# Kernel tuning notes

Measured on AMD Instinct MI355X. Metric: run time of the kernel, lower is better.

Reference implementation:

```python
import jax, jax.numpy as jnp
import numpy as np

B, M, S, E, LC, V, HOPS = 16, 2048, 6, 128, 512, 32000, 3
PAD = 1


def setup_inputs() -> dict:
    key = jax.random.key(0)
    ks = jax.random.split(key, 16)
    story = jax.random.randint(ks[0], (B, M, S), 0, V)
    kb_len = jax.random.randint(ks[1], (B,), 0, M - LC)
    conv_len = jax.random.randint(ks[2], (B,), 0, LC)
    hidden = jax.random.normal(ks[3], (1, B, 2 * E), jnp.float32)
    dh_outputs = jax.random.normal(ks[4], (B, LC, E), jnp.float32)
    tf_hidden = jax.random.normal(ks[5], (B, E), jnp.float32)
    query_vector = jax.random.normal(ks[6], (B, E), jnp.float32)
    global_pointer = jax.random.uniform(ks[7], (B, M), jnp.float32)
    C = jax.random.normal(ks[8], (HOPS + 1, V, E), jnp.float32) * 0.1
    C = C.at[:, PAD, :].set(0.0)  # padding_idx row is zero
    s = 0.05
    wA1 = jax.random.normal(ks[9], (2 * E, E), jnp.float32) * s
    bA1 = jnp.zeros((E,), jnp.float32)
    wA2 = jax.random.normal(ks[10], (E, E), jnp.float32) * s
    bA2 = jnp.zeros((E,), jnp.float32)
    wC1 = jax.random.normal(ks[11], (2 * E, E), jnp.float32) * s
    bC1 = jnp.zeros((E,), jnp.float32)
    wC2 = jax.random.normal(ks[12], (E, E), jnp.float32) * s
    bC2 = jnp.zeros((E,), jnp.float32)
    wf = jax.random.normal(ks[13], (2 * E, E), jnp.float32) * s
    bf = jnp.zeros((E,), jnp.float32)
    return dict(story=story, kb_len=kb_len, conv_len=conv_len, hidden=hidden,
                dh_outputs=dh_outputs, tf_hidden=tf_hidden, query_vector=query_vector,
                global_pointer=global_pointer, C=C, wA1=wA1, bA1=bA1, wA2=wA2, bA2=bA2,
                wC1=wC1, bC1=bC1, wC2=wC2, bC2=bC2, wf=wf, bf=bf)


def _lrelu(x):
    return jnp.where(x > 0, x, 0.1 * x)  # LeakyReLU(0.1)


def _mlp(x, w1, b1, w2, b2):
    return _lrelu(x @ w1 + b1) @ w2 + b2


def _add_lm(mem, kb_len, conv_len, dh):
    # mem: [B,M,E]; add dh[bi,:conv_len[bi]] into rows [kb_len, kb_len+conv_len)
    pos = jnp.arange(mem.shape[1])[None, :]            # [1,M]
    idx = pos - kb_len[:, None]                        # [B,M]
    mask = (idx >= 0) & (idx < conv_len[:, None])
    gathered = jnp.take_along_axis(dh, jnp.clip(idx, 0, dh.shape[1] - 1)[..., None], axis=1)
    return mem + jnp.where(mask[..., None], gathered, 0.0)


def reference(story, kb_len, conv_len, hidden, dh_outputs, tf_hidden,
              query_vector, global_pointer, C, wA1, bA1, wA2, bA2,
              wC1, bC1, wC2, bC2, wf, bf):
    # --- load_ent_memory: build m_story_ent (dropout off / eval mode) ---
    u = _lrelu(hidden[0] @ wf + bf)                    # hidden.squeeze(0) -> [B,E]
    tf = jnp.broadcast_to(tf_hidden[:, None, :], (B, M, E))
    m_story = []
    eC = None
    for hop in range(HOPS):
        eA = _add_lm(C[hop][story].sum(2), kb_len, conv_len, dh_outputs)       # [B,M,E]
        eA = _mlp(jnp.concatenate([eA, tf], -1), wA1, bA1, wA2, bA2)
        logit = jnp.einsum('bme,be->bm', eA, u)
        p = jax.nn.softmax(logit, axis=1)
        eC = _add_lm(C[hop + 1][story].sum(2), kb_len, conv_len, dh_outputs)   # [B,M,E]
        eC = _mlp(jnp.concatenate([eC, tf], -1), wC1, bC1, wC2, bC2)
        u = u + jnp.einsum('bme,bm->be', eC, p)
        m_story.append(eA)
    m_story.append(eC)
    # --- forward(query_vector, global_pointer) ---
    uq = query_vector
    gp = global_pointer[..., None]                     # [B,M,1]
    prob_logits = None
    prob_soft = None
    for hop in range(HOPS):
        mA = m_story[hop] * gp
        prob_logits = jnp.einsum('bme,be->bm', mA, uq)
        prob_soft = jax.nn.softmax(prob_logits, axis=1)
        mC = m_story[hop + 1] * gp
        uq = uq + jnp.einsum('bme,bm->be', mC, prob_soft)
    return (prob_soft, prob_logits)
```

## Files before the change

kernel.cpp:

```cpp
#include <hip/hip_runtime.h>
#include <math.h>

#define BB 16
#define MM 2048
#define SS 6
#define EE 128
#define LCC 512
#define VV 32000

typedef __attribute__((ext_vector_type(8))) __bf16 bf16x8;
typedef __attribute__((ext_vector_type(4))) float f32x4;

#define XS_STRIDE 264
#define HS_STRIDE 136

static __device__ inline unsigned short bfbits(float x) {
    __bf16 h = (__bf16)x;
    return __builtin_bit_cast(unsigned short, h);
}

#define N_W1  (256 * 128)
#define N_W2  (128 * 128)
#define N_UQ  (BB * EE)
#define N_PREP (N_W1 + N_W2 + 2 * N_UQ)

__global__ __launch_bounds__(256)
void prep_small(const float* __restrict__ W1, const float* __restrict__ W2,
                __bf16* __restrict__ w1t, __bf16* __restrict__ w2t,
                float* __restrict__ uqA, float* __restrict__ uqB)
{
    int i = blockIdx.x * 256 + threadIdx.x;
    if (i < N_W1) { const int n = i >> 8, k = i & 255; w1t[i] = (__bf16)W1[k * EE + n]; return; }
    i -= N_W1;
    if (i < N_W2) { const int n = i >> 7, k = i & 127; w2t[i] = (__bf16)W2[k * EE + n]; return; }
    i -= N_W2;
    if (i < N_UQ) { uqA[i] = 0.f; return; }
    i -= N_UQ;
    if (i < N_UQ) { uqB[i] = 0.f; }
}

__global__ __launch_bounds__(256)
void embed_mlp_mfma(const int* __restrict__ story,
                    const int* __restrict__ kb_len,
                    const int* __restrict__ conv_len,
                    const float* __restrict__ dh,
                    const float* __restrict__ tf,
                    const float* __restrict__ C,
                    const __bf16* __restrict__ w1t, const float* __restrict__ b1,
                    const __bf16* __restrict__ w2t, const float* __restrict__ b2,
                    const float* __restrict__ gp, const float* __restrict__ query,
                    __bf16* __restrict__ mout, float* __restrict__ lbuf0)
{
    __shared__ __bf16 Xs[32 * XS_STRIDE];
    __shared__ int    sidx[32 * SS];
    __bf16* Hs   = Xs;
    float*  plog = (float*)Xs;

    const int bid  = blockIdx.x;
    const int hop  = bid >> 10;
    const int row0 = (bid & 1023) * 32;
    const int b    = row0 >> 11;
    const int tid  = threadIdx.x;

    const float* Ck = C + (size_t)hop * VV * EE;

    for (int i = tid; i < 32 * SS; i += 256) sidx[i] = story[(size_t)row0 * SS + i];

    const int kb   = kb_len[b];
    const int cl   = conv_len[b];
    const int rgrp = tid >> 5;
    const int e4   = (tid & 31) * 4;
    const float4 tf4 = *(const float4*)&tf[b * EE + e4];
    ushort4 tfp;
    tfp.x = bfbits(tf4.x); tfp.y = bfbits(tf4.y); tfp.z = bfbits(tf4.z); tfp.w = bfbits(tf4.w);
    __syncthreads();

    for (int chunk = 0; chunk < 4; ++chunk) {
        const int r  = chunk * 8 + rgrp;
        const int* si = &sidx[r * SS];
        float4 v[SS];
        #pragma unroll
        for (int s = 0; s < SS; ++s)
            v[s] = *(const float4*)&Ck[(size_t)si[s] * EE + e4];
        const int j = ((row0 + r) & (MM - 1)) - kb;
        float4 acc = {0.f, 0.f, 0.f, 0.f};
        if (j >= 0 && j < cl)
            acc = *(const float4*)&dh[((size_t)b * LCC + j) * EE + e4];
        #pragma unroll
        for (int s = 0; s < SS; ++s) {
            acc.x += v[s].x; acc.y += v[s].y; acc.z += v[s].z; acc.w += v[s].w;
        }
        ushort4 pk;
        pk.x = bfbits(acc.x); pk.y = bfbits(acc.y); pk.z = bfbits(acc.z); pk.w = bfbits(acc.w);
        *(ushort4*)&Xs[r * XS_STRIDE + e4]      = pk;
        *(ushort4*)&Xs[r * XS_STRIDE + EE + e4] = tfp;
    }
    __syncthreads();

    const int w       = tid >> 6;
    const int lane    = tid & 63;
    const int lr      = lane & 15;
    const int lk      = lane >> 4;
    const int colbase = w * 32;

    f32x4 acc1[2][2];
    #pragma unroll
    for (int i = 0; i < 2; ++i)
        #pragma unroll
        for (int j = 0; j < 2; ++j) acc1[i][j] = (f32x4){0.f, 0.f, 0.f, 0.f};

    for (int ks = 0; ks < 8; ++ks) {
        bf16x8 a[2], bw[2];
        #pragma unroll
        for (int mt = 0; mt < 2; ++mt)
            a[mt] = *(const bf16x8*)&Xs[(mt * 16 + lr) * XS_STRIDE + ks * 32 + lk * 8];
        #pragma unroll
        for (int nt = 0; nt < 2; ++nt)
            bw[nt] = *(const bf16x8*)&w1t[(size_t)(colbase + nt * 16 + lr) * 256 + ks * 32 + lk * 8];
        #pragma unroll
        for (int mt = 0; mt < 2; ++mt)
            #pragma unroll
            for (int nt = 0; nt < 2; ++nt)
                acc1[mt][nt] = __builtin_amdgcn_mfma_f32_16x16x32_bf16(a[mt], bw[nt], acc1[mt][nt], 0, 0, 0);
    }
    __syncthreads();
    {
        const float b1v[2] = { b1[colbase + lr], b1[colbase + 16 + lr] };
        #pragma unroll
        for (int mt = 0; mt < 2; ++mt)
            #pragma unroll
            for (int nt = 0; nt < 2; ++nt)
                #pragma unroll
                for (int reg = 0; reg < 4; ++reg) {
                    float h = acc1[mt][nt][reg] + b1v[nt];
                    h = (h > 0.f) ? h : 0.1f * h;
                    Hs[(mt * 16 + lk * 4 + reg) * HS_STRIDE + colbase + nt * 16 + lr] = (__bf16)h;
                }
    }
    __syncthreads();

    f32x4 acc2[2][2];
    #pragma unroll
    for (int i = 0; i < 2; ++i)
        #pragma unroll
        for (int j = 0; j < 2; ++j) acc2[i][j] = (f32x4){0.f, 0.f, 0.f, 0.f};

    for (int ks = 0; ks < 4; ++ks) {
        bf16x8 a[2], bw[2];
        #pragma unroll
        for (int mt = 0; mt < 2; ++mt)
            a[mt] = *(const bf16x8*)&Hs[(mt * 16 + lr) * HS_STRIDE + ks * 32 + lk * 8];
        #pragma unroll
        for (int nt = 0; nt < 2; ++nt)
            bw[nt] = *(const bf16x8*)&w2t[(size_t)(colbase + nt * 16 + lr) * 128 + ks * 32 + lk * 8];
        #pragma unroll
        for (int mt = 0; mt < 2; ++mt)
            #pragma unroll
            for (int nt = 0; nt < 2; ++nt)
                acc2[mt][nt] = __builtin_amdgcn_mfma_f32_16x16x32_bf16(a[mt], bw[nt], acc2[mt][nt], 0, 0, 0);
    }

    const float b2v[2] = { b2[colbase + lr], b2[colbase + 16 + lr] };

    if (hop == 0) {
        const float qv0 = query[b * EE + colbase + lr];
        const float qv1 = query[b * EE + colbase + 16 + lr];
        __syncthreads();
        #pragma unroll
        for (int mt = 0; mt < 2; ++mt)
            #pragma unroll
            for (int reg = 0; reg < 4; ++reg) {
                float p = (acc2[mt][0][reg] + b2v[0]) * qv0
                        + (acc2[mt][1][reg] + b2v[1]) * qv1;
                p += __shfl_xor(p, 1, 64);
                p += __shfl_xor(p, 2, 64);
                p += __shfl_xor(p, 4, 64);
                p += __shfl_xor(p, 8, 64);
                if (lr == 0) plog[(mt * 16 + lk * 4 + reg) * 4 + w] = p;
            }
        __syncthreads();
        if (tid < 32) {
            const float l = plog[tid * 4] + plog[tid * 4 + 1] + plog[tid * 4 + 2] + plog[tid * 4 + 3];
            lbuf0[row0 + tid] = l * gp[row0 + tid];
        }
    } else {
        __bf16* out = mout + (size_t)(hop - 1) * 32768 * EE;
        #pragma unroll
        for (int mt = 0; mt < 2; ++mt)
            #pragma unroll
            for (int nt = 0; nt < 2; ++nt)
                #pragma unroll
                for (int reg = 0; reg < 4; ++reg) {
                    const int rg_ = row0 + mt * 16 + lk * 4 + reg;
                    out[(size_t)rg_ * EE + colbase + nt * 16 + lr] =
                        (__bf16)(acc2[mt][nt][reg] + b2v[nt]);
                }
    }
}

__global__ __launch_bounds__(256)
void update_kernel(const __bf16* __restrict__ mk, const float* __restrict__ gp,
                   const float* __restrict__ lbuf, float* __restrict__ uq)
{
    __shared__ float redm[4], reds[4];
    __shared__ float wls[64];
    __shared__ float part[4][128];

    const int b      = blockIdx.x >> 5;
    const int rloc0  = (blockIdx.x & 31) * 64;
    const int tid    = threadIdx.x;
    const int lane   = tid & 63;
    const int w      = tid >> 6;
    const float* lb  = lbuf + (size_t)b * MM;

    float v[8];
    float mx = -1e30f;
    #pragma unroll
    for (int i = 0; i < 8; ++i) { v[i] = lb[i * 256 + tid]; mx = fmaxf(mx, v[i]); }
    #pragma unroll
    for (int off = 32; off > 0; off >>= 1) mx = fmaxf(mx, __shfl_xor(mx, off, 64));
    if (lane == 0) redm[w] = mx;
    __syncthreads();
    mx = fmaxf(fmaxf(redm[0], redm[1]), fmaxf(redm[2], redm[3]));
    float sum = 0.f;
    #pragma unroll
    for (int i = 0; i < 8; ++i) sum += __expf(v[i] - mx);
    #pragma unroll
    for (int off = 32; off > 0; off >>= 1) sum += __shfl_xor(sum, off, 64);
    if (lane == 0) reds[w] = sum;
    __syncthreads();
    const float inv = 1.f / (reds[0] + reds[1] + reds[2] + reds[3]);

    if (tid < 64)
        wls[tid] = gp[(size_t)b * MM + rloc0 + tid] * __expf(lb[rloc0 + tid] - mx) * inv;
    __syncthreads();

    const int rgrp = tid >> 4;
    const int e8   = (tid & 15) * 8;
    float acc[8];
    #pragma unroll
    for (int q = 0; q < 8; ++q) acc[q] = 0.f;
    #pragma unroll
    for (int p = 0; p < 4; ++p) {
        const int rl  = p * 16 + rgrp;
        const float wg = wls[rl];
        const bf16x8 vv = *(const bf16x8*)&mk[((size_t)b * MM + rloc0 + rl) * EE + e8];
        #pragma unroll
        for (int q = 0; q < 8; ++q) acc[q] += wg * (float)vv[q];
    }
    #pragma unroll
    for (int q = 0; q < 8; ++q) {
        acc[q] += __shfl_xor(acc[q], 16, 64);
        acc[q] += __shfl_xor(acc[q], 32, 64);
    }
    if (lane < 16) {
        #pragma unroll
        for (int q = 0; q < 8; ++q) part[w][e8 + q] = acc[q];
    }
    __syncthreads();
    if (tid < 128) {
        const float s = part[0][tid] + part[1][tid] + part[2][tid] + part[3][tid];
        atomicAdd(&uq[b * EE + tid], s);
    }
}

__global__ __launch_bounds__(256)
void logits_kernel(const __bf16* __restrict__ mk, const float* __restrict__ gp,
                   const float* __restrict__ query, const float* __restrict__ uqa,
                   const float* __restrict__ uqb, float* __restrict__ out)
{
    __shared__ float uqs[128];
    const int row0 = blockIdx.x * 64;
    const int b    = row0 >> 11;
    const int tid  = threadIdx.x;
    if (tid < 128)
        uqs[tid] = query[b * EE + tid] + uqa[b * EE + tid]
                 + (uqb ? uqb[b * EE + tid] : 0.f);
    __syncthreads();
    const int w = tid >> 6, lane = tid & 63;
    const int g = lane >> 4, l16 = lane & 15;
    float u[8];
    #pragma unroll
    for (int j = 0; j < 8; ++j) u[j] = uqs[l16 * 8 + j];
    #pragma unroll
    for (int it = 0; it < 4; ++it) {
        const int row = row0 + it * 16 + w * 4 + g;
        const bf16x8 v = *(const bf16x8*)&mk[(size_t)row * EE + l16 * 8];
        float p = 0.f;
        #pragma unroll
        for (int j = 0; j < 8; ++j) p += (float)v[j] * u[j];
        p += __shfl_xor(p, 1, 64);
        p += __shfl_xor(p, 2, 64);
        p += __shfl_xor(p, 4, 64);
        p += __shfl_xor(p, 8, 64);
        if (l16 == 0) out[row] = p * gp[row];
    }
}

__global__ __launch_bounds__(256)
void softmax_final(const float* __restrict__ logits, float* __restrict__ soft)
{
    __shared__ float redm[4], reds[4];
    const int b = blockIdx.x, tid = threadIdx.x;
    const int lane = tid & 63, w = tid >> 6;
    const float* lb = logits + (size_t)b * MM;
    float v[8];
    float mx = -1e30f;
    #pragma unroll
    for (int i = 0; i < 8; ++i) { v[i] = lb[i * 256 + tid]; mx = fmaxf(mx, v[i]); }
    #pragma unroll
    for (int off = 32; off > 0; off >>= 1) mx = fmaxf(mx, __shfl_xor(mx, off, 64));
    if (lane == 0) redm[w] = mx;
    __syncthreads();
    mx = fmaxf(fmaxf(redm[0], redm[1]), fmaxf(redm[2], redm[3]));
    float sum = 0.f;
    #pragma unroll
    for (int i = 0; i < 8; ++i) { v[i] = __expf(v[i] - mx); sum += v[i]; }
    #pragma unroll
    for (int off = 32; off > 0; off >>= 1) sum += __shfl_xor(sum, off, 64);
    if (lane == 0) reds[w] = sum;
    __syncthreads();
    const float inv = 1.f / (reds[0] + reds[1] + reds[2] + reds[3]);
    #pragma unroll
    for (int i = 0; i < 8; ++i) soft[(size_t)b * MM + i * 256 + tid] = v[i] * inv;
}

extern "C" void kernel_launch(void* const* d_in, const int* in_sizes, int n_in,
                              void* d_out, int out_size, void* d_ws, size_t ws_size,
                              hipStream_t stream) {
    const int*   story    = (const int*)d_in[0];
    const int*   kb_len   = (const int*)d_in[1];
    const int*   conv_len = (const int*)d_in[2];
    const float* dh       = (const float*)d_in[4];
    const float* tf       = (const float*)d_in[5];
    const float* query    = (const float*)d_in[6];
    const float* gp       = (const float*)d_in[7];
    const float* C        = (const float*)d_in[8];
    const float* wA1      = (const float*)d_in[9];
    const float* bA1      = (const float*)d_in[10];
    const float* wA2      = (const float*)d_in[11];
    const float* bA2      = (const float*)d_in[12];

    char* ws = (char*)d_ws;
    const size_t M_ELEMS = (size_t)32768 * EE;
    size_t off = 0;
    __bf16* m   = (__bf16*)(ws + off); off += 2 * M_ELEMS * sizeof(__bf16);
    __bf16* w1t = (__bf16*)(ws + off); off += 256 * 128 * sizeof(__bf16);
    __bf16* w2t = (__bf16*)(ws + off); off += 128 * 128 * sizeof(__bf16);
    float* lbuf = (float*)(ws + off);  off += (size_t)BB * MM * sizeof(float);
    float* uqA  = (float*)(ws + off);  off += (size_t)BB * EE * sizeof(float);
    float* uqB  = (float*)(ws + off);  off += (size_t)BB * EE * sizeof(float);

    float* out_soft   = (float*)d_out;
    float* out_logits = out_soft + (size_t)BB * MM;

    prep_small<<<N_PREP / 256, 256, 0, stream>>>(wA1, wA2, w1t, w2t, uqA, uqB);
    embed_mlp_mfma<<<3072, 256, 0, stream>>>(story, kb_len, conv_len, dh, tf, C,
                                             w1t, bA1, w2t, bA2, gp, query, m, lbuf);
    update_kernel<<<512, 256, 0, stream>>>(m, gp, lbuf, uqA);
    logits_kernel<<<512, 256, 0, stream>>>(m, gp, query, uqA, nullptr, lbuf);
    update_kernel<<<512, 256, 0, stream>>>(m + M_ELEMS, gp, lbuf, uqB);
    logits_kernel<<<512, 256, 0, stream>>>(m + M_ELEMS, gp, query, uqA, uqB, out_logits);
    softmax_final<<<BB, 256, 0, stream>>>(out_logits, out_soft);
}
```

Measured before the change: 193.1 us.

## Fuse tail update/logits/softmax launches into one cooperative kernel with grid syncs

Replaces the five small tail kernels (two update, two logits, final softmax) with a single cooperative kernel of 512 blocks that separates the phases with grid-wide barriers. The goal is to remove the launch gaps between these short kernels. The final softmax is now computed redundantly by every block, each writing 64 outputs, instead of by 16 blocks. The cost is grid-sync latency and reliance on all 512 blocks being co-resident.

```diff
diff --git a/kernel.cpp b/kernel.cpp
--- a/kernel.cpp
+++ b/kernel.cpp
@@ -1,5 +1,8 @@
 #include <hip/hip_runtime.h>
+#include <hip/hip_cooperative_groups.h>
 #include <math.h>
+
+namespace cg = cooperative_groups;
 
 #define BB 16
 #define MM 2048
@@ -198,21 +201,13 @@
     }
 }
 
-__global__ __launch_bounds__(256)
-void update_kernel(const __bf16* __restrict__ mk, const float* __restrict__ gp,
-                   const float* __restrict__ lbuf, float* __restrict__ uq)
+static __device__ inline void update_phase(
+    const __bf16* __restrict__ mk, const float* __restrict__ gp,
+    const float* __restrict__ lbuf, float* __restrict__ uq,
+    int b, int rloc0, int tid, int lane, int w,
+    float* redm, float* reds, float* wls, float (*part)[128])
 {
-    __shared__ float redm[4], reds[4];
-    __shared__ float wls[64];
-    __shared__ float part[4][128];
-
-    const int b      = blockIdx.x >> 5;
-    const int rloc0  = (blockIdx.x & 31) * 64;
-    const int tid    = threadIdx.x;
-    const int lane   = tid & 63;
-    const int w      = tid >> 6;
-    const float* lb  = lbuf + (size_t)b * MM;
-
+    const float* lb = lbuf + (size_t)b * MM;
     float v[8];
     float mx = -1e30f;
     #pragma unroll
@@ -264,20 +259,17 @@
     }
 }
 
-__global__ __launch_bounds__(256)
-void logits_kernel(const __bf16* __restrict__ mk, const float* __restrict__ gp,
-                   const float* __restrict__ query, const float* __restrict__ uqa,
-                   const float* __restrict__ uqb, float* __restrict__ out)
+static __device__ inline void logits_phase(
+    const __bf16* __restrict__ mk, const float* __restrict__ gp,
+    const float* __restrict__ query, const float* __restrict__ uqa,
+    const float* __restrict__ uqb, float* __restrict__ out,
+    int bid, int b, int tid, int lane, int w, float* uqs)
 {
-    __shared__ float uqs[128];
-    const int row0 = blockIdx.x * 64;
-    const int b    = row0 >> 11;
-    const int tid  = threadIdx.x;
+    const int row0 = bid * 64;
     if (tid < 128)
         uqs[tid] = query[b * EE + tid] + uqa[b * EE + tid]
                  + (uqb ? uqb[b * EE + tid] : 0.f);
     __syncthreads();
-    const int w = tid >> 6, lane = tid & 63;
     const int g = lane >> 4, l16 = lane & 15;
     float u[8];
     #pragma unroll
@@ -295,34 +287,70 @@
         p += __shfl_xor(p, 8, 64);
         if (l16 == 0) out[row] = p * gp[row];
     }
+    __syncthreads();
 }
 
 __global__ __launch_bounds__(256)
-void softmax_final(const float* __restrict__ logits, float* __restrict__ soft)
+void fused_tail(const __bf16* __restrict__ mall, const float* __restrict__ gp,
+                const float* __restrict__ query, float* __restrict__ lbuf,
+                float* __restrict__ uqA, float* __restrict__ uqB,
+                float* __restrict__ out_logits, float* __restrict__ out_soft)
 {
+    cg::grid_group grid = cg::this_grid();
     __shared__ float redm[4], reds[4];
-    const int b = blockIdx.x, tid = threadIdx.x;
-    const int lane = tid & 63, w = tid >> 6;
-    const float* lb = logits + (size_t)b * MM;
-    float v[8];
-    float mx = -1e30f;
-    #pragma unroll
-    for (int i = 0; i < 8; ++i) { v[i] = lb[i * 256 + tid]; mx = fmaxf(mx, v[i]); }
-    #pragma unroll
-    for (int off = 32; off > 0; off >>= 1) mx = fmaxf(mx, __shfl_xor(mx, off, 64));
-    if (lane == 0) redm[w] = mx;
-    __syncthreads();
-    mx = fmaxf(fmaxf(redm[0], redm[1]), fmaxf(redm[2], redm[3]));
-    float sum = 0.f;
-    #pragma unroll
-    for (int i = 0; i < 8; ++i) { v[i] = __expf(v[i] - mx); sum += v[i]; }
-    #pragma unroll
-    for (int off = 32; off > 0; off >>= 1) sum += __shfl_xor(sum, off, 64);
-    if (lane == 0) reds[w] = sum;
-    __syncthreads();
-    const float inv = 1.f / (reds[0] + reds[1] + reds[2] + reds[3]);
-    #pragma unroll
-    for (int i = 0; i < 8; ++i) soft[(size_t)b * MM + i * 256 + tid] = v[i] * inv;
+    __shared__ float wls[64];
+    __shared__ float part[4][128];
+    __shared__ float uqs[128];
+
+    const int bid   = blockIdx.x;
+    const int b     = bid >> 5;
+    const int rloc0 = (bid & 31) * 64;
+    const int tid   = threadIdx.x;
+    const int lane  = tid & 63;
+    const int w     = tid >> 6;
+
+    const __bf16* m1 = mall;
+    const __bf16* m2 = mall + (size_t)32768 * EE;
+
+    update_phase(m1, gp, lbuf, uqA, b, rloc0, tid, lane, w, redm, reds, wls, part);
+    __threadfence();
+    grid.sync();
+
+    logits_phase(m1, gp, query, uqA, nullptr, lbuf, bid, b, tid, lane, w, uqs);
+    __threadfence();
+    grid.sync();
+
+    update_phase(m2, gp, lbuf, uqB, b, rloc0, tid, lane, w, redm, reds, wls, part);
+    __threadfence();
+    grid.sync();
+
+    logits_phase(m2, gp, query, uqA, uqB, out_logits, bid, b, tid, lane, w, uqs);
+    __threadfence();
+    grid.sync();
+
+    {
+        const float* lb = out_logits + (size_t)b * MM;
+        float v[8];
+        float mx = -1e30f;
+        #pragma unroll
+        for (int i = 0; i < 8; ++i) { v[i] = lb[i * 256 + tid]; mx = fmaxf(mx, v[i]); }
+        #pragma unroll
+        for (int off = 32; off > 0; off >>= 1) mx = fmaxf(mx, __shfl_xor(mx, off, 64));
+        if (lane == 0) redm[w] = mx;
+        __syncthreads();
+        mx = fmaxf(fmaxf(redm[0], redm[1]), fmaxf(redm[2], redm[3]));
+        float sum = 0.f;
+        #pragma unroll
+        for (int i = 0; i < 8; ++i) sum += __expf(v[i] - mx);
+        #pragma unroll
+        for (int off = 32; off > 0; off >>= 1) sum += __shfl_xor(sum, off, 64);
+        if (lane == 0) reds[w] = sum;
+        __syncthreads();
+        const float inv = 1.f / (reds[0] + reds[1] + reds[2] + reds[3]);
+        if (tid < 64)
+            out_soft[(size_t)b * MM + rloc0 + tid] =
+                __expf(lb[rloc0 + tid] - mx) * inv;
+    }
 }
 
 extern "C" void kernel_launch(void* const* d_in, const int* in_sizes, int n_in,
@@ -357,9 +385,16 @@
     prep_small<<<N_PREP / 256, 256, 0, stream>>>(wA1, wA2, w1t, w2t, uqA, uqB);
     embed_mlp_mfma<<<3072, 256, 0, stream>>>(story, kb_len, conv_len, dh, tf, C,
                                              w1t, bA1, w2t, bA2, gp, query, m, lbuf);
-    update_kernel<<<512, 256, 0, stream>>>(m, gp, lbuf, uqA);
-    logits_kernel<<<512, 256, 0, stream>>>(m, gp, query, uqA, nullptr, lbuf);
-    update_kernel<<<512, 256, 0, stream>>>(m + M_ELEMS, gp, lbuf, uqB);
-    logits_kernel<<<512, 256, 0, stream>>>(m + M_ELEMS, gp, query, uqA, uqB, out_logits);
-    softmax_final<<<BB, 256, 0, stream>>>(out_logits, out_soft);
-}
+
+    const __bf16* marg = m;
+    const float*  gparg = gp;
+    const float*  qarg  = query;
+    float* lbarg = lbuf;
+    float* uaarg = uqA;
+    float* ubarg = uqB;
+    float* olarg = out_logits;
+    float* osarg = out_soft;
+    void* args[] = { (void*)&marg, (void*)&gparg, (void*)&qarg, (void*)&lbarg,
+                     (void*)&uaarg, (void*)&ubarg, (void*)&olarg, (void*)&osarg };
+    hipLaunchCooperativeKernel(fused_tail, dim3(512), dim3(256), args, 0u, stream);
+}
```

Result: slower. 548.0 us (+183.8%).

## Fuse update, logits and final softmax into one per-batch tail kernel

Applied to the files above, without the earlier changes.

Replaces the five tail launches (two update, two logits, final softmax) with a single kernel that runs one 1024-thread block per batch. Softmax weights, the u-vector reduction, the logits and the final softmax all stay in shared memory, so the atomics, the uq zeroing and the intermediate global round-trips go away. The cost is parallelism: only 16 blocks stream 2×16×2048×128 bf16 values, each read twice, which could leave most of the chip idle and make the tail bandwidth-bound on a few CUs.

```diff
diff --git a/kernel.cpp b/kernel.cpp
--- a/kernel.cpp
+++ b/kernel.cpp
@@ -21,22 +21,16 @@
 
 #define N_W1  (256 * 128)
 #define N_W2  (128 * 128)
-#define N_UQ  (BB * EE)
-#define N_PREP (N_W1 + N_W2 + 2 * N_UQ)
+#define N_PREP (N_W1 + N_W2)
 
 __global__ __launch_bounds__(256)
 void prep_small(const float* __restrict__ W1, const float* __restrict__ W2,
-                __bf16* __restrict__ w1t, __bf16* __restrict__ w2t,
-                float* __restrict__ uqA, float* __restrict__ uqB)
+                __bf16* __restrict__ w1t, __bf16* __restrict__ w2t)
 {
     int i = blockIdx.x * 256 + threadIdx.x;
     if (i < N_W1) { const int n = i >> 8, k = i & 255; w1t[i] = (__bf16)W1[k * EE + n]; return; }
     i -= N_W1;
-    if (i < N_W2) { const int n = i >> 7, k = i & 127; w2t[i] = (__bf16)W2[k * EE + n]; return; }
-    i -= N_W2;
-    if (i < N_UQ) { uqA[i] = 0.f; return; }
-    i -= N_UQ;
-    if (i < N_UQ) { uqB[i] = 0.f; }
+    if (i < N_W2) { const int n = i >> 7, k = i & 127; w2t[i] = (__bf16)W2[k * EE + n]; }
 }
 
 __global__ __launch_bounds__(256)
@@ -198,53 +192,49 @@
     }
 }
 
-__global__ __launch_bounds__(256)
-void update_kernel(const __bf16* __restrict__ mk, const float* __restrict__ gp,
-                   const float* __restrict__ lbuf, float* __restrict__ uq)
-{
-    __shared__ float redm[4], reds[4];
-    __shared__ float wls[64];
-    __shared__ float part[4][128];
-
-    const int b      = blockIdx.x >> 5;
-    const int rloc0  = (blockIdx.x & 31) * 64;
-    const int tid    = threadIdx.x;
-    const int lane   = tid & 63;
-    const int w      = tid >> 6;
-    const float* lb  = lbuf + (size_t)b * MM;
-
-    float v[8];
-    float mx = -1e30f;
-    #pragma unroll
-    for (int i = 0; i < 8; ++i) { v[i] = lb[i * 256 + tid]; mx = fmaxf(mx, v[i]); }
+static __device__ inline void softmax_weights(
+    const float* __restrict__ src, const float* __restrict__ gls,
+    float* __restrict__ wls, float* redm, float* reds,
+    int tid, int wv, int lane)
+{
+    const float v0 = src[tid], v1 = src[tid + 1024];
+    float mx = fmaxf(v0, v1);
     #pragma unroll
     for (int off = 32; off > 0; off >>= 1) mx = fmaxf(mx, __shfl_xor(mx, off, 64));
-    if (lane == 0) redm[w] = mx;
-    __syncthreads();
-    mx = fmaxf(fmaxf(redm[0], redm[1]), fmaxf(redm[2], redm[3]));
-    float sum = 0.f;
-    #pragma unroll
-    for (int i = 0; i < 8; ++i) sum += __expf(v[i] - mx);
+    if (lane == 0) redm[wv] = mx;
+    __syncthreads();
+    mx = redm[0];
+    #pragma unroll
+    for (int k = 1; k < 16; ++k) mx = fmaxf(mx, redm[k]);
+    const float e0 = __expf(v0 - mx), e1 = __expf(v1 - mx);
+    float sum = e0 + e1;
     #pragma unroll
     for (int off = 32; off > 0; off >>= 1) sum += __shfl_xor(sum, off, 64);
-    if (lane == 0) reds[w] = sum;
-    __syncthreads();
-    const float inv = 1.f / (reds[0] + reds[1] + reds[2] + reds[3]);
-
-    if (tid < 64)
-        wls[tid] = gp[(size_t)b * MM + rloc0 + tid] * __expf(lb[rloc0 + tid] - mx) * inv;
-    __syncthreads();
-
+    if (lane == 0) reds[wv] = sum;
+    __syncthreads();
+    float tot = reds[0];
+    #pragma unroll
+    for (int k = 1; k < 16; ++k) tot += reds[k];
+    const float inv = 1.f / tot;
+    wls[tid]        = gls[tid]        * e0 * inv;
+    wls[tid + 1024] = gls[tid + 1024] * e1 * inv;
+    __syncthreads();
+}
+
+static __device__ inline void update_u(
+    const __bf16* __restrict__ mk, const float* __restrict__ wls,
+    float (*part)[128], float* __restrict__ ured,
+    int tid, int wv, int lane)
+{
     const int rgrp = tid >> 4;
     const int e8   = (tid & 15) * 8;
     float acc[8];
     #pragma unroll
     for (int q = 0; q < 8; ++q) acc[q] = 0.f;
-    #pragma unroll
-    for (int p = 0; p < 4; ++p) {
-        const int rl  = p * 16 + rgrp;
-        const float wg = wls[rl];
-        const bf16x8 vv = *(const bf16x8*)&mk[((size_t)b * MM + rloc0 + rl) * EE + e8];
+    for (int p = 0; p < 32; ++p) {
+        const int r = p * 64 + rgrp;
+        const float wg = wls[r];
+        const bf16x8 vv = *(const bf16x8*)&mk[(size_t)r * EE + e8];
         #pragma unroll
         for (int q = 0; q < 8; ++q) acc[q] += wg * (float)vv[q];
     }
@@ -255,36 +245,29 @@
     }
     if (lane < 16) {
         #pragma unroll
-        for (int q = 0; q < 8; ++q) part[w][e8 + q] = acc[q];
+        for (int q = 0; q < 8; ++q) part[wv][lane * 8 + q] = acc[q];
     }
     __syncthreads();
     if (tid < 128) {
-        const float s = part[0][tid] + part[1][tid] + part[2][tid] + part[3][tid];
-        atomicAdd(&uq[b * EE + tid], s);
-    }
-}
-
-__global__ __launch_bounds__(256)
-void logits_kernel(const __bf16* __restrict__ mk, const float* __restrict__ gp,
-                   const float* __restrict__ query, const float* __restrict__ uqa,
-                   const float* __restrict__ uqb, float* __restrict__ out)
-{
-    __shared__ float uqs[128];
-    const int row0 = blockIdx.x * 64;
-    const int b    = row0 >> 11;
-    const int tid  = threadIdx.x;
-    if (tid < 128)
-        uqs[tid] = query[b * EE + tid] + uqa[b * EE + tid]
-                 + (uqb ? uqb[b * EE + tid] : 0.f);
-    __syncthreads();
-    const int w = tid >> 6, lane = tid & 63;
+        float s = 0.f;
+        #pragma unroll
+        for (int k = 0; k < 16; ++k) s += part[k][tid];
+        ured[tid] += s;
+    }
+    __syncthreads();
+}
+
+static __device__ inline void logits_u(
+    const __bf16* __restrict__ mk, const float* __restrict__ gls,
+    const float* __restrict__ uvec, float* __restrict__ slog,
+    int tid, int wv, int lane)
+{
     const int g = lane >> 4, l16 = lane & 15;
     float u[8];
     #pragma unroll
-    for (int j = 0; j < 8; ++j) u[j] = uqs[l16 * 8 + j];
-    #pragma unroll
-    for (int it = 0; it < 4; ++it) {
-        const int row = row0 + it * 16 + w * 4 + g;
+    for (int j = 0; j < 8; ++j) u[j] = uvec[l16 * 8 + j];
+    for (int it = 0; it < 32; ++it) {
+        const int row = it * 64 + wv * 4 + g;
         const bf16x8 v = *(const bf16x8*)&mk[(size_t)row * EE + l16 * 8];
         float p = 0.f;
         #pragma unroll
@@ -293,36 +276,73 @@
         p += __shfl_xor(p, 2, 64);
         p += __shfl_xor(p, 4, 64);
         p += __shfl_xor(p, 8, 64);
-        if (l16 == 0) out[row] = p * gp[row];
-    }
-}
-
-__global__ __launch_bounds__(256)
-void softmax_final(const float* __restrict__ logits, float* __restrict__ soft)
-{
-    __shared__ float redm[4], reds[4];
-    const int b = blockIdx.x, tid = threadIdx.x;
-    const int lane = tid & 63, w = tid >> 6;
-    const float* lb = logits + (size_t)b * MM;
-    float v[8];
-    float mx = -1e30f;
-    #pragma unroll
-    for (int i = 0; i < 8; ++i) { v[i] = lb[i * 256 + tid]; mx = fmaxf(mx, v[i]); }
+        if (l16 == 0) slog[row] = p * gls[row];
+    }
+    __syncthreads();
+}
+
+__global__ __launch_bounds__(1024)
+void tail_kernel(const __bf16* __restrict__ mall, const float* __restrict__ gp,
+                 const float* __restrict__ query, const float* __restrict__ lbuf0,
+                 float* __restrict__ out_logits, float* __restrict__ out_soft)
+{
+    __shared__ float gls[2048];
+    __shared__ float wls[2048];
+    __shared__ float slog[2048];
+    __shared__ float part[16][128];
+    __shared__ float ured[128];
+    __shared__ float uvec[128];
+    __shared__ float redm[16], reds[16];
+
+    const int b    = blockIdx.x;
+    const int tid  = threadIdx.x;
+    const int wv   = tid >> 6;
+    const int lane = tid & 63;
+
+    const __bf16* m1 = mall + (size_t)b * MM * EE;
+    const __bf16* m2 = mall + (size_t)32768 * EE + (size_t)b * MM * EE;
+
+    gls[tid]        = gp[(size_t)b * MM + tid];
+    gls[tid + 1024] = gp[(size_t)b * MM + tid + 1024];
+    if (tid < 128) ured[tid] = 0.f;
+    __syncthreads();
+
+    softmax_weights(lbuf0 + (size_t)b * MM, gls, wls, redm, reds, tid, wv, lane);
+    update_u(m1, wls, part, ured, tid, wv, lane);
+    if (tid < 128) uvec[tid] = query[b * EE + tid] + ured[tid];
+    __syncthreads();
+    logits_u(m1, gls, uvec, slog, tid, wv, lane);
+
+    softmax_weights(slog, gls, wls, redm, reds, tid, wv, lane);
+    update_u(m2, wls, part, ured, tid, wv, lane);
+    if (tid < 128) uvec[tid] = query[b * EE + tid] + ured[tid];
+    __syncthreads();
+    logits_u(m2, gls, uvec, slog, tid, wv, lane);
+
+    const float l0 = slog[tid], l1 = slog[tid + 1024];
+    out_logits[(size_t)b * MM + tid]        = l0;
+    out_logits[(size_t)b * MM + tid + 1024] = l1;
+
+    float mx = fmaxf(l0, l1);
     #pragma unroll
     for (int off = 32; off > 0; off >>= 1) mx = fmaxf(mx, __shfl_xor(mx, off, 64));
-    if (lane == 0) redm[w] = mx;
-    __syncthreads();
-    mx = fmaxf(fmaxf(redm[0], redm[1]), fmaxf(redm[2], redm[3]));
-    float sum = 0.f;
-    #pragma unroll
-    for (int i = 0; i < 8; ++i) { v[i] = __expf(v[i] - mx); sum += v[i]; }
+    if (lane == 0) redm[wv] = mx;
+    __syncthreads();
+    mx = redm[0];
+    #pragma unroll
+    for (int k = 1; k < 16; ++k) mx = fmaxf(mx, redm[k]);
+    const float e0 = __expf(l0 - mx), e1 = __expf(l1 - mx);
+    float sum = e0 + e1;
     #pragma unroll
     for (int off = 32; off > 0; off >>= 1) sum += __shfl_xor(sum, off, 64);
-    if (lane == 0) reds[w] = sum;
-    __syncthreads();
-    const float inv = 1.f / (reds[0] + reds[1] + reds[2] + reds[3]);
-    #pragma unroll
-    for (int i = 0; i < 8; ++i) soft[(size_t)b * MM + i * 256 + tid] = v[i] * inv;
+    if (lane == 0) reds[wv] = sum;
+    __syncthreads();
+    float tot = reds[0];
+    #pragma unroll
+    for (int k = 1; k < 16; ++k) tot += reds[k];
+    const float inv = 1.f / tot;
+    out_soft[(size_t)b * MM + tid]        = e0 * inv;
+    out_soft[(size_t)b * MM + tid + 1024] = e1 * inv;
 }
 
 extern "C" void kernel_launch(void* const* d_in, const int* in_sizes, int n_in,
@@ -348,18 +368,12 @@
     __bf16* w1t = (__bf16*)(ws + off); off += 256 * 128 * sizeof(__bf16);
     __bf16* w2t = (__bf16*)(ws + off); off += 128 * 128 * sizeof(__bf16);
     float* lbuf = (float*)(ws + off);  off += (size_t)BB * MM * sizeof(float);
-    float* uqA  = (float*)(ws + off);  off += (size_t)BB * EE * sizeof(float);
-    float* uqB  = (float*)(ws + off);  off += (size_t)BB * EE * sizeof(float);
 
     float* out_soft   = (float*)d_out;
     float* out_logits = out_soft + (size_t)BB * MM;
 
-    prep_small<<<N_PREP / 256, 256, 0, stream>>>(wA1, wA2, w1t, w2t, uqA, uqB);
+    prep_small<<<N_PREP / 256, 256, 0, stream>>>(wA1, wA2, w1t, w2t);
     embed_mlp_mfma<<<3072, 256, 0, stream>>>(story, kb_len, conv_len, dh, tf, C,
                                              w1t, bA1, w2t, bA2, gp, query, m, lbuf);
-    update_kernel<<<512, 256, 0, stream>>>(m, gp, lbuf, uqA);
-    logits_kernel<<<512, 256, 0, stream>>>(m, gp, query, uqA, nullptr, lbuf);
-    update_kernel<<<512, 256, 0, stream>>>(m + M_ELEMS, gp, lbuf, uqB);
-    logits_kernel<<<512, 256, 0, stream>>>(m + M_ELEMS, gp, query, uqA, uqB, out_logits);
-    softmax_final<<<BB, 256, 0, stream>>>(out_logits, out_soft);
-}
+    tail_kernel<<<BB, 1024, 0, stream>>>(m, gp, query, lbuf, out_logits, out_soft);
+}
```

New measurement: 212.5 us. 1.1x slower.
